# Optimization experiments

Measured on AMD Instinct MI355X. Metric: run time of the kernel, lower is better.

Reference implementation:

```python
import jax, jax.numpy as jnp
import numpy as np

N_NODES = 32768
N_EDGES = 524288
IN_CH = 128
OUT_CH = 128
EDGE_CH = 64
HIDDEN = 128


def setup_inputs() -> dict:
    key = jax.random.key(0)
    ks = jax.random.split(key, 8)
    x = jax.random.normal(ks[0], (N_NODES, IN_CH), dtype=jnp.float32)
    edge_index = jax.random.randint(ks[1], (2, N_EDGES), 0, N_NODES, dtype=jnp.int64)
    edge_attr = jax.random.uniform(ks[2], (N_EDGES, EDGE_CH), dtype=jnp.float32)
    # filter_network: Linear(edge_ch, hidden) -> tanh -> Linear(hidden, out)
    s1 = 1.0 / np.sqrt(EDGE_CH)
    s2 = 1.0 / np.sqrt(HIDDEN)
    W1 = jax.random.uniform(ks[3], (EDGE_CH, HIDDEN), jnp.float32, -s1, s1)
    b1 = jax.random.uniform(ks[4], (HIDDEN,), jnp.float32, -s1, s1)
    W2 = jax.random.uniform(ks[5], (HIDDEN, OUT_CH), jnp.float32, -s2, s2)
    b2 = jax.random.uniform(ks[6], (OUT_CH,), jnp.float32, -s2, s2)
    # attention_vector [out, 1], xavier_uniform with gain 1.414
    lim = 1.414 * np.sqrt(6.0 / (OUT_CH + 1))
    attn = jax.random.uniform(ks[7], (OUT_CH,), jnp.float32, -lim, lim)
    return {"x": x, "edge_index": edge_index, "edge_attr": edge_attr,
            "W1": W1, "b1": b1, "W2": W2, "b2": b2, "attn": attn}


def _segment_softmax(scores, segment_ids, num_segments):
    # PyG-style numerically stable softmax over segments
    seg_max = jax.ops.segment_max(scores, segment_ids, num_segments=num_segments)
    seg_max = jnp.where(jnp.isfinite(seg_max), seg_max, 0.0)
    e = jnp.exp(scores - seg_max[segment_ids])
    denom = jax.ops.segment_sum(e, segment_ids, num_segments=num_segments)
    return e / (denom[segment_ids] + 1e-16)


def reference(x, edge_index, edge_attr, W1, b1, W2, b2, attn):
    source, target = edge_index[0], edge_index[1]
    n_nodes = x.shape[0]
    source_features = x[source]                                  # [E, in]
    edge_attr_norm = edge_attr / (jnp.linalg.norm(edge_attr, axis=-1, keepdims=True) + 1e-8)
    h = jnp.tanh(edge_attr_norm @ W1 + b1)                       # [E, hidden]
    edge_filters = h @ W2 + b2                                   # [E, out]
    messages = source_features * edge_filters                    # [E, out]
    attention_scores = messages @ attn                           # [E]
    attention_weights = _segment_softmax(attention_scores, target, n_nodes)
    messages = messages * attention_weights[:, None]
    output = jax.ops.segment_sum(messages, target, num_segments=n_nodes)  # [N, out]
    return output, attention_weights
```

## Files before the change

### kernel.cpp

```cpp
#include <hip/hip_runtime.h>
#include <stdint.h>

typedef short short8 __attribute__((ext_vector_type(8)));
typedef float f32x16 __attribute__((ext_vector_type(16)));
typedef unsigned ux4 __attribute__((ext_vector_type(4)));

__device__ __forceinline__ unsigned cvtpk(float lo, float hi){
  unsigned r;
  asm("v_cvt_pk_bf16_f32 %0, %1, %2" : "=v"(r) : "v"(lo), "v"(hi));
  return r;
}

__device__ __forceinline__ short8 frag_from(unsigned a, unsigned b, unsigned c, unsigned d){
  union { unsigned u[4]; short8 s; } t;
  t.u[0] = a; t.u[1] = b; t.u[2] = c; t.u[3] = d;
  return t.s;
}

__global__ void k_prep(const float* __restrict__ W1, const float* __restrict__ W2,
                       ux4* __restrict__ Wf)
{
  const int t = blockIdx.x * 256 + threadIdx.x;
  if (t >= 48 * 64) return;
  const int f = t >> 6, l = t & 63;
  const int r = l & 31, hh = l >> 5;
  float v[8];
  if (f < 16) {
    const int mf = f >> 2, ks = f & 3;
    const int c = 32 * mf + r, kb = ks * 16 + hh * 8;
#pragma unroll
    for (int j = 0; j < 8; ++j) v[j] = W1[(kb + j) * 128 + c];
  } else {
    const int f2 = f - 16, mf2 = f2 >> 3, ks = f2 & 7;
    const int o = 32 * mf2 + r, cb = ks * 16 + hh * 8;
#pragma unroll
    for (int j = 0; j < 8; ++j) v[j] = W2[(cb + j) * 128 + o];
  }
  ux4 d;
  d.x = cvtpk(v[0], v[1]); d.y = cvtpk(v[2], v[3]);
  d.z = cvtpk(v[4], v[5]); d.w = cvtpk(v[6], v[7]);
  Wf[(long long)f * 64 + l] = d;
}

__global__ void k_setup(const float* __restrict__ x, uint2* __restrict__ xb, int n4,
                        const int* __restrict__ ei, int* __restrict__ rowptr, int E)
{
  const long long tot = (n4 > E) ? n4 : E;
  for (long long i = (long long)blockIdx.x * 256 + threadIdx.x; i < tot;
       i += (long long)gridDim.x * 256) {
    if (i < n4) {
      float4 v = ((const float4*)x)[i];
      uint2 o; o.x = cvtpk(v.x, v.y); o.y = cvtpk(v.z, v.w);
      xb[i] = o;
    }
    if (i < E) atomicAdd(&rowptr[ei[E + i]], 1);
  }
}

__global__ __launch_bounds__(1024)
void k_scan(int* __restrict__ p, int N){
  __shared__ int ls[1024];
  const int t = threadIdx.x;
  const int chunk = (N + 1023) >> 10;
  const int c0 = t * chunk, c1 = min(N, c0 + chunk);
  int s = 0;
  for (int i = c0; i < c1; ++i) s += p[i];
  ls[t] = s;
  __syncthreads();
  for (int off = 1; off < 1024; off <<= 1) {
    int add = (t >= off) ? ls[t - off] : 0;
    __syncthreads();
    ls[t] += add;
    __syncthreads();
  }
  int run = (t == 0) ? 0 : ls[t - 1];
  for (int i = c0; i < c1; ++i) { int v = p[i]; p[i] = run; run += v; }
}

__global__ void k_fill(const int* __restrict__ ei, int* __restrict__ rowptr,
                       int* __restrict__ pose, int* __restrict__ eidx, int E){
  for (long long i = (long long)blockIdx.x * 256 + threadIdx.x; i < E;
       i += (long long)gridDim.x * 256) {
    int tg = ei[E + i];
    int pos = atomicAdd(&rowptr[tg], 1);
    pose[i] = pos;
    eidx[pos] = (int)i;
  }
}

#define K1B 512
__global__ __launch_bounds__(K1B)
void k1_fused(const unsigned* __restrict__ xb, const int* __restrict__ ei,
              const float* __restrict__ ea, const ux4* __restrict__ Wf,
              const float* __restrict__ b1, const float* __restrict__ b2,
              const float* __restrict__ attn, const int* __restrict__ eidx,
              unsigned* __restrict__ msgp, float* __restrict__ scoreS, int E)
{
  __shared__ ux4 sWf[48 * 64];
  for (int i = threadIdx.x; i < 48 * 64; i += K1B) sWf[i] = Wf[i];
  __syncthreads();

  const int lane = threadIdx.x & 63;
  const int wv   = threadIdx.x >> 6;
  const int h    = lane >> 5;
  const int r31  = lane & 31;
  const long long gstep = (long long)gridDim.x * (K1B / 64) * 32;
  long long p = ((long long)blockIdx.x * (K1B / 64) + wv) * 32 + r31;
  if (p - r31 >= E) return;

  int eC = eidx[(p < E) ? p : (long long)(E - 1)];
  int srcC = ei[eC];
  unsigned ebC[4][4]; float rinC;
  {
    const float* er = ea + (long long)eC * 64 + h * 8;
    float4 v[8];
#pragma unroll
    for (int ks = 0; ks < 4; ++ks) {
      v[2*ks]   = *(const float4*)(er + ks * 16);
      v[2*ks+1] = *(const float4*)(er + ks * 16 + 4);
    }
    float ss = 0.f;
#pragma unroll
    for (int k8 = 0; k8 < 8; ++k8) {
      ss = fmaf(v[k8].x, v[k8].x, ss); ss = fmaf(v[k8].y, v[k8].y, ss);
      ss = fmaf(v[k8].z, v[k8].z, ss); ss = fmaf(v[k8].w, v[k8].w, ss);
    }
    ss += __shfl_xor(ss, 32);
    rinC = 1.0f / (sqrtf(ss) + 1e-8f);
#pragma unroll
    for (int ks = 0; ks < 4; ++ks) {
      ebC[ks][0] = cvtpk(v[2*ks].x,   v[2*ks].y);
      ebC[ks][1] = cvtpk(v[2*ks].z,   v[2*ks].w);
      ebC[ks][2] = cvtpk(v[2*ks+1].x, v[2*ks+1].y);
      ebC[ks][3] = cvtpk(v[2*ks+1].z, v[2*ks+1].w);
    }
  }
  long long pn = p + gstep;
  bool hasN = (pn - r31) < E;
  int eN = 0;
  if (hasN) eN = eidx[(pn < E) ? pn : (long long)(E - 1)];

  while (true) {
    float4 eaN[8]; int srcN = 0;
    if (hasN) {
      srcN = ei[eN];
      const float* er = ea + (long long)eN * 64 + h * 8;
#pragma unroll
      for (int ks = 0; ks < 4; ++ks) {
        eaN[2*ks]   = *(const float4*)(er + ks * 16);
        eaN[2*ks+1] = *(const float4*)(er + ks * 16 + 4);
      }
    }
    long long pnn = pn + gstep;
    bool hasNN = hasN && ((pnn - r31) < E);
    int eNN = 0;
    if (hasNN) eNN = eidx[(pnn < E) ? pnn : (long long)(E - 1)];

    const unsigned* xrow = xb + (long long)srcC * 64;
    uint2 xw[4];
#pragma unroll
    for (int rq = 0; rq < 4; ++rq)
      xw[rq] = *(const uint2*)(xrow + (8*rq + 4*h) / 2);
    asm volatile("" ::: "memory");

    unsigned hb[8][4];
#pragma unroll
    for (int mf = 0; mf < 4; ++mf) {
      f32x16 a1;
#pragma unroll
      for (int i = 0; i < 16; ++i) a1[i] = 0.f;
#pragma unroll
      for (int ks = 0; ks < 4; ++ks) {
        ux4 w = sWf[(mf * 4 + ks) * 64 + lane];
        a1 = __builtin_amdgcn_mfma_f32_32x32x16_bf16(
            frag_from(w.x, w.y, w.z, w.w),
            frag_from(ebC[ks][0], ebC[ks][1], ebC[ks][2], ebC[ks][3]), a1, 0, 0, 0);
      }
      float hv[16];
#pragma unroll
      for (int rq = 0; rq < 4; ++rq) {
        float4 bc = *(const float4*)(b1 + 32*mf + 8*rq + 4*h);
#pragma unroll
        for (int i = 0; i < 4; ++i) {
          float pre = fmaf(a1[rq*4+i], rinC, ((const float*)&bc)[i]);
          float e2  = __expf(2.0f * pre);
          hv[rq*4+i] = 1.0f - 2.0f / (e2 + 1.0f);
        }
      }
#pragma unroll
      for (int q = 0; q < 2; ++q) {
        unsigned A = cvtpk(hv[q*8+0], hv[q*8+1]);
        unsigned B = cvtpk(hv[q*8+2], hv[q*8+3]);
        unsigned C = cvtpk(hv[q*8+4], hv[q*8+5]);
        unsigned D = cvtpk(hv[q*8+6], hv[q*8+7]);
        unsigned Axr = (unsigned)__shfl_xor((int)A, 32);
        unsigned Bxr = (unsigned)__shfl_xor((int)B, 32);
        unsigned Cxr = (unsigned)__shfl_xor((int)C, 32);
        unsigned Dxr = (unsigned)__shfl_xor((int)D, 32);
        hb[2*mf+q][0] = h ? Cxr : A;
        hb[2*mf+q][1] = h ? Dxr : B;
        hb[2*mf+q][2] = h ? C   : Axr;
        hb[2*mf+q][3] = h ? D   : Bxr;
      }
    }

    float score = 0.f;
#pragma unroll
    for (int mf2 = 0; mf2 < 4; ++mf2) {
      uint2 xwN[4];
      if (mf2 < 3) {
#pragma unroll
        for (int rq = 0; rq < 4; ++rq)
          xwN[rq] = *(const uint2*)(xrow + (32*(mf2+1) + 8*rq + 4*h) / 2);
      }
      f32x16 a2;
#pragma unroll
      for (int i = 0; i < 16; ++i) a2[i] = 0.f;
#pragma unroll
      for (int ks = 0; ks < 8; ++ks) {
        ux4 w = sWf[(16 + mf2 * 8 + ks) * 64 + lane];
        a2 = __builtin_amdgcn_mfma_f32_32x32x16_bf16(
            frag_from(w.x, w.y, w.z, w.w),
            frag_from(hb[ks][0], hb[ks][1], hb[ks][2], hb[ks][3]), a2, 0, 0, 0);
      }
      unsigned pk[8];
#pragma unroll
      for (int rq = 0; rq < 4; ++rq) {
        const int o0 = 32*mf2 + 8*rq + 4*h;
        float4 b2c = *(const float4*)(b2 + o0);
        float4 atc = *(const float4*)(attn + o0);
        float x0 = __uint_as_float(xw[rq].x << 16);
        float x1 = __uint_as_float(xw[rq].x & 0xffff0000u);
        float x2 = __uint_as_float(xw[rq].y << 16);
        float x3 = __uint_as_float(xw[rq].y & 0xffff0000u);
        float m0 = (a2[rq*4+0] + b2c.x) * x0;
        float m1 = (a2[rq*4+1] + b2c.y) * x1;
        float m2 = (a2[rq*4+2] + b2c.z) * x2;
        float m3 = (a2[rq*4+3] + b2c.w) * x3;
        score = fmaf(m0, atc.x, score);
        score = fmaf(m1, atc.y, score);
        score = fmaf(m2, atc.z, score);
        score = fmaf(m3, atc.w, score);
        pk[2*rq]   = cvtpk(m0, m1);
        pk[2*rq+1] = cvtpk(m2, m3);
      }
      if (p < E) {
        ux4* dst = (ux4*)(msgp + p * 64 + 16*mf2 + 8*h);
        ux4 s0, s1;
        s0.x = pk[0]; s0.y = pk[1]; s0.z = pk[2]; s0.w = pk[3];
        s1.x = pk[4]; s1.y = pk[5]; s1.z = pk[6]; s1.w = pk[7];
        dst[0] = s0; dst[1] = s1;
      }
      if (mf2 < 3) {
#pragma unroll
        for (int rq = 0; rq < 4; ++rq) xw[rq] = xwN[rq];
      }
    }
    score += __shfl_xor(score, 32);
    if (h == 0 && p < E) scoreS[p] = score;

    if (!hasN) break;
    float ss = 0.f;
#pragma unroll
    for (int k8 = 0; k8 < 8; ++k8) {
      ss = fmaf(eaN[k8].x, eaN[k8].x, ss); ss = fmaf(eaN[k8].y, eaN[k8].y, ss);
      ss = fmaf(eaN[k8].z, eaN[k8].z, ss); ss = fmaf(eaN[k8].w, eaN[k8].w, ss);
    }
    ss += __shfl_xor(ss, 32);
    rinC = 1.0f / (sqrtf(ss) + 1e-8f);
#pragma unroll
    for (int ks = 0; ks < 4; ++ks) {
      ebC[ks][0] = cvtpk(eaN[2*ks].x,   eaN[2*ks].y);
      ebC[ks][1] = cvtpk(eaN[2*ks].z,   eaN[2*ks].w);
      ebC[ks][2] = cvtpk(eaN[2*ks+1].x, eaN[2*ks+1].y);
      ebC[ks][3] = cvtpk(eaN[2*ks+1].z, eaN[2*ks+1].w);
    }
    srcC = srcN; p = pn; pn = pnn; hasN = hasNN; eN = eNN;
  }
}

__global__ __launch_bounds__(256)
void k_gather(const unsigned* __restrict__ msgp, const float* __restrict__ scoreS,
              const int* __restrict__ rowptr, float* __restrict__ lse,
              float* __restrict__ out, int N)
{
  const int lane = threadIdx.x & 63;
  const int node = blockIdx.x * 4 + (threadIdx.x >> 6);
  if (node >= N) return;
  const int end   = rowptr[node];
  const int start = node ? rowptr[node - 1] : 0;
  const int L     = end - start;

  float m = -3.4e38f, s = 0.f;
  for (int c0 = 0; c0 < L; c0 += 64) {
    const int j = c0 + lane;
    float sc = (j < L) ? scoreS[start + j] : -3.4e38f;
    float cm = sc;
#pragma unroll
    for (int off = 32; off; off >>= 1) cm = fmaxf(cm, __shfl_xor(cm, off));
    const float mn = fmaxf(m, cm);
    float ex = (j < L) ? __expf(sc - mn) : 0.f;
#pragma unroll
    for (int off = 32; off; off >>= 1) ex += __shfl_xor(ex, off);
    s = s * __expf(m - mn) + ex;
    m = mn;
  }
  const float lsev = m + logf(s + 1e-16f);
  if (lane == 0) lse[node] = lsev;

  float2 acc; acc.x = 0.f; acc.y = 0.f;
  for (int c0 = 0; c0 < L; c0 += 64) {
    const int j = c0 + lane;
    float w = (j < L) ? __expf(scoreS[start + j] - lsev) : 0.f;
    const int jn = min(64, L - c0);
#pragma unroll 4
    for (int j2 = 0; j2 < jn; ++j2) {
      float wj = __shfl(w, j2);
      unsigned md = msgp[(long long)(start + c0 + j2) * 64 + lane];
      acc.x = fmaf(wj, __uint_as_float(md << 16),          acc.x);
      acc.y = fmaf(wj, __uint_as_float(md & 0xffff0000u), acc.y);
    }
  }
  const int mf2 = lane >> 4, hh = (lane >> 3) & 1, rq = (lane >> 1) & 3, half = lane & 1;
  const int ch0 = 32*mf2 + 8*rq + 4*hh + 2*half;
  *(float2*)(out + (long long)node * 128 + ch0) = acc;
}

__global__ void k_wfin(int* __restrict__ pw, const int* __restrict__ ei,
                       const float* __restrict__ scoreS, const float* __restrict__ lse,
                       int E){
  for (long long i = (long long)blockIdx.x * 256 + threadIdx.x; i < E;
       i += (long long)gridDim.x * 256) {
    int pos = pw[i];
    float w = __expf(scoreS[pos] - lse[ei[E + i]]);
    pw[i] = __float_as_int(w);
  }
}

extern "C" void kernel_launch(void* const* d_in, const int* in_sizes, int n_in,
                              void* d_out, int out_size, void* d_ws, size_t ws_size,
                              hipStream_t stream)
{
  const float* x    = (const float*)d_in[0];
  const int*   ei   = (const int*)d_in[1];
  const float* ea   = (const float*)d_in[2];
  const float* W1   = (const float*)d_in[3];
  const float* b1   = (const float*)d_in[4];
  const float* W2   = (const float*)d_in[5];
  const float* b2   = (const float*)d_in[6];
  const float* attn = (const float*)d_in[7];
  const int N = in_sizes[0] / 128;
  const int E = in_sizes[2] / 64;
  if (E <= 0 || N <= 0) return;

  float* out   = (float*)d_out;
  float* wregN = out + (long long)N * 128;
  ux4*     Wf   = (ux4*)d_out;
  size_t   offE = 65536;
  int*     eidx = (int*)((char*)d_out + offE);
  size_t   offX = (offE + (size_t)E * 4 + 255) & ~(size_t)255;
  unsigned* xb  = (unsigned*)((char*)d_out + offX);

  char* wsb = (char*)d_ws;
  unsigned* msgp   = (unsigned*)wsb;
  float*    scoreS = (float*)(wsb + (size_t)E * 256);
  int*      rowptr = (int*)(wsb + (size_t)E * 256 + (size_t)E * 4);
  float*    lse    = (float*)(wsb + (size_t)E * 260 + (size_t)N * 4);
  const size_t need = (size_t)E * 260 + (size_t)N * 8;
  if (ws_size < need) return;
  if ((size_t)out_size < (size_t)N * 128 + (size_t)E) return;
  if ((size_t)N * 512 < offX + (size_t)N * 256) return;

  (void)hipMemsetAsync(rowptr, 0, (size_t)N * 4, stream);
  k_prep<<<12, 256, 0, stream>>>(W1, W2, Wf);
  k_setup<<<1024, 256, 0, stream>>>(x, (uint2*)xb, N * 32, ei, rowptr, E);
  k_scan<<<1, 1024, 0, stream>>>(rowptr, N);
  k_fill<<<1024, 256, 0, stream>>>(ei, rowptr, (int*)wregN, eidx, E);
  const long long nwaves = ((long long)E + 31) / 32;
  const int grid = (int)min((long long)512, (nwaves + (K1B/64) - 1) / (K1B/64));
  k1_fused<<<grid, K1B, 0, stream>>>(xb, ei, ea, Wf, b1, b2, attn,
                                     eidx, msgp, scoreS, E);
  k_gather<<<(N + 3) / 4, 256, 0, stream>>>(msgp, scoreS, rowptr, lse, out, N);
  k_wfin<<<1024, 256, 0, stream>>>((int*)wregN, ei, scoreS, lse, E);
}
```

Baseline: 277.8 us.

## Fold weight prep into setup, deepen x prefetch, raise MFMA wave priority

The weight-fragment prep kernel is merged into k_setup, which removes one kernel launch. In the fused edge kernel, the source-feature bf16 row is now loaded two column blocks ahead into a 16-entry register array instead of being double-buffered one block ahead. The MFMA loops are wrapped in s_setprio(1)/s_setprio(0) so that waves issuing matrix instructions get priority. The deeper prefetch raises register pressure and may lower occupancy.

```diff
diff --git a/kernel.cpp b/kernel.cpp
--- a/kernel.cpp
+++ b/kernel.cpp
@@ -17,37 +17,34 @@
   return t.s;
 }
 
-__global__ void k_prep(const float* __restrict__ W1, const float* __restrict__ W2,
-                       ux4* __restrict__ Wf)
+__global__ void k_setup(const float* __restrict__ x, uint2* __restrict__ xb, int n4,
+                        const int* __restrict__ ei, int* __restrict__ rowptr, int E,
+                        const float* __restrict__ W1, const float* __restrict__ W2,
+                        ux4* __restrict__ Wf)
 {
-  const int t = blockIdx.x * 256 + threadIdx.x;
-  if (t >= 48 * 64) return;
-  const int f = t >> 6, l = t & 63;
-  const int r = l & 31, hh = l >> 5;
-  float v[8];
-  if (f < 16) {
-    const int mf = f >> 2, ks = f & 3;
-    const int c = 32 * mf + r, kb = ks * 16 + hh * 8;
-#pragma unroll
-    for (int j = 0; j < 8; ++j) v[j] = W1[(kb + j) * 128 + c];
-  } else {
-    const int f2 = f - 16, mf2 = f2 >> 3, ks = f2 & 7;
-    const int o = 32 * mf2 + r, cb = ks * 16 + hh * 8;
-#pragma unroll
-    for (int j = 0; j < 8; ++j) v[j] = W2[(cb + j) * 128 + o];
-  }
-  ux4 d;
-  d.x = cvtpk(v[0], v[1]); d.y = cvtpk(v[2], v[3]);
-  d.z = cvtpk(v[4], v[5]); d.w = cvtpk(v[6], v[7]);
-  Wf[(long long)f * 64 + l] = d;
-}
-
-__global__ void k_setup(const float* __restrict__ x, uint2* __restrict__ xb, int n4,
-                        const int* __restrict__ ei, int* __restrict__ rowptr, int E)
-{
+  const long long tid = (long long)blockIdx.x * 256 + threadIdx.x;
+  if (tid < 48 * 64) {
+    const int f = (int)(tid >> 6), l = (int)(tid & 63);
+    const int r = l & 31, hh = l >> 5;
+    float v[8];
+    if (f < 16) {
+      const int mf = f >> 2, ks = f & 3;
+      const int c = 32 * mf + r, kb = ks * 16 + hh * 8;
+#pragma unroll
+      for (int j = 0; j < 8; ++j) v[j] = W1[(kb + j) * 128 + c];
+    } else {
+      const int f2 = f - 16, mf2 = f2 >> 3, ks = f2 & 7;
+      const int o = 32 * mf2 + r, cb = ks * 16 + hh * 8;
+#pragma unroll
+      for (int j = 0; j < 8; ++j) v[j] = W2[(cb + j) * 128 + o];
+    }
+    ux4 d;
+    d.x = cvtpk(v[0], v[1]); d.y = cvtpk(v[2], v[3]);
+    d.z = cvtpk(v[4], v[5]); d.w = cvtpk(v[6], v[7]);
+    Wf[(long long)f * 64 + l] = d;
+  }
   const long long tot = (n4 > E) ? n4 : E;
-  for (long long i = (long long)blockIdx.x * 256 + threadIdx.x; i < tot;
-       i += (long long)gridDim.x * 256) {
+  for (long long i = tid; i < tot; i += (long long)gridDim.x * 256) {
     if (i < n4) {
       float4 v = ((const float4*)x)[i];
       uint2 o; o.x = cvtpk(v.x, v.y); o.y = cvtpk(v.z, v.w);
@@ -157,10 +154,12 @@
     if (hasNN) eNN = eidx[(pnn < E) ? pnn : (long long)(E - 1)];
 
     const unsigned* xrow = xb + (long long)srcC * 64;
-    uint2 xw[4];
-#pragma unroll
-    for (int rq = 0; rq < 4; ++rq)
-      xw[rq] = *(const uint2*)(xrow + (8*rq + 4*h) / 2);
+    uint2 xw[16];
+#pragma unroll
+    for (int i = 0; i < 8; ++i) {
+      const int mf2 = i >> 2, rq = i & 3;
+      xw[i] = *(const uint2*)(xrow + (32*mf2 + 8*rq + 4*h) / 2);
+    }
     asm volatile("" ::: "memory");
 
     unsigned hb[8][4];
@@ -169,6 +168,7 @@
       f32x16 a1;
 #pragma unroll
       for (int i = 0; i < 16; ++i) a1[i] = 0.f;
+      __builtin_amdgcn_s_setprio(1);
 #pragma unroll
       for (int ks = 0; ks < 4; ++ks) {
         ux4 w = sWf[(mf * 4 + ks) * 64 + lane];
@@ -176,6 +176,7 @@
             frag_from(w.x, w.y, w.z, w.w),
             frag_from(ebC[ks][0], ebC[ks][1], ebC[ks][2], ebC[ks][3]), a1, 0, 0, 0);
       }
+      __builtin_amdgcn_s_setprio(0);
       float hv[16];
 #pragma unroll
       for (int rq = 0; rq < 4; ++rq) {
@@ -207,15 +208,15 @@
     float score = 0.f;
 #pragma unroll
     for (int mf2 = 0; mf2 < 4; ++mf2) {
-      uint2 xwN[4];
-      if (mf2 < 3) {
+      if (mf2 < 2) {
 #pragma unroll
         for (int rq = 0; rq < 4; ++rq)
-          xwN[rq] = *(const uint2*)(xrow + (32*(mf2+1) + 8*rq + 4*h) / 2);
+          xw[(mf2+2)*4+rq] = *(const uint2*)(xrow + (32*(mf2+2) + 8*rq + 4*h) / 2);
       }
       f32x16 a2;
 #pragma unroll
       for (int i = 0; i < 16; ++i) a2[i] = 0.f;
+      __builtin_amdgcn_s_setprio(1);
 #pragma unroll
       for (int ks = 0; ks < 8; ++ks) {
         ux4 w = sWf[(16 + mf2 * 8 + ks) * 64 + lane];
@@ -223,16 +224,18 @@
             frag_from(w.x, w.y, w.z, w.w),
             frag_from(hb[ks][0], hb[ks][1], hb[ks][2], hb[ks][3]), a2, 0, 0, 0);
       }
+      __builtin_amdgcn_s_setprio(0);
       unsigned pk[8];
 #pragma unroll
       for (int rq = 0; rq < 4; ++rq) {
         const int o0 = 32*mf2 + 8*rq + 4*h;
         float4 b2c = *(const float4*)(b2 + o0);
         float4 atc = *(const float4*)(attn + o0);
-        float x0 = __uint_as_float(xw[rq].x << 16);
-        float x1 = __uint_as_float(xw[rq].x & 0xffff0000u);
-        float x2 = __uint_as_float(xw[rq].y << 16);
-        float x3 = __uint_as_float(xw[rq].y & 0xffff0000u);
+        uint2 xc = xw[mf2*4+rq];
+        float x0 = __uint_as_float(xc.x << 16);
+        float x1 = __uint_as_float(xc.x & 0xffff0000u);
+        float x2 = __uint_as_float(xc.y << 16);
+        float x3 = __uint_as_float(xc.y & 0xffff0000u);
         float m0 = (a2[rq*4+0] + b2c.x) * x0;
         float m1 = (a2[rq*4+1] + b2c.y) * x1;
         float m2 = (a2[rq*4+2] + b2c.z) * x2;
@@ -250,10 +253,6 @@
         s0.x = pk[0]; s0.y = pk[1]; s0.z = pk[2]; s0.w = pk[3];
         s1.x = pk[4]; s1.y = pk[5]; s1.z = pk[6]; s1.w = pk[7];
         dst[0] = s0; dst[1] = s1;
-      }
-      if (mf2 < 3) {
-#pragma unroll
-        for (int rq = 0; rq < 4; ++rq) xw[rq] = xwN[rq];
       }
     }
     score += __shfl_xor(score, 32);
@@ -372,8 +371,7 @@
   if ((size_t)N * 512 < offX + (size_t)N * 256) return;
 
   (void)hipMemsetAsync(rowptr, 0, (size_t)N * 4, stream);
-  k_prep<<<12, 256, 0, stream>>>(W1, W2, Wf);
-  k_setup<<<1024, 256, 0, stream>>>(x, (uint2*)xb, N * 32, ei, rowptr, E);
+  k_setup<<<1024, 256, 0, stream>>>(x, (uint2*)xb, N * 32, ei, rowptr, E, W1, W2, Wf);
   k_scan<<<1, 1024, 0, stream>>>(rowptr, N);
   k_fill<<<1024, 256, 0, stream>>>(ei, rowptr, (int*)wregN, eidx, E);
   const long long nwaves = ((long long)E + 31) / 32;
```

Result: slower. 284.2 us (+2.3%).
